# Kernel tuning notes

Measured on AMD Instinct MI355X. Metric: run time of the kernel, lower is better.

The kernel has to match this reference:

```python
import jax, jax.numpy as jnp
import numpy as np

N_NODES = 100000


def gcn_conv(x, W, b, src, dst, n_nodes):
    # x: [N, Fin], W: [Fin, Fout], edge (src->dst) with self-loops added,
    # symmetric normalization D^{-1/2} A D^{-1/2} as in PyG GCNConv defaults.
    h = x @ W  # [N, Fout]
    loops = jnp.arange(n_nodes, dtype=src.dtype)
    src_all = jnp.concatenate([src, loops])
    dst_all = jnp.concatenate([dst, loops])
    ones = jnp.ones(src_all.shape[0], dtype=h.dtype)
    deg = jax.ops.segment_sum(ones, dst_all, num_segments=n_nodes)  # in-degree incl. self-loop
    dinv = jnp.where(deg > 0, jax.lax.rsqrt(deg), 0.0)
    norm = dinv[src_all] * dinv[dst_all]  # [E+N]
    msg = h[src_all] * norm[:, None]      # gather + scale
    out = jax.ops.segment_sum(msg, dst_all, num_segments=n_nodes)  # scatter-add
    return out + b


def setup_inputs() -> dict:
    key = jax.random.key(0)
    k1, k2, k3, k4 = jax.random.split(key, 4)
    in_dim, hidden, out_dim = 128, 128, 64
    n_edges = 600000
    x = jax.random.normal(k1, (N_NODES, in_dim), dtype=jnp.float32)
    edge_index = jax.random.randint(k2, (2, n_edges), 0, N_NODES, dtype=jnp.int64)
    # Glorot-ish init for weights
    W1 = jax.random.normal(k3, (in_dim, hidden), dtype=jnp.float32) / np.sqrt(in_dim)
    b1 = jnp.zeros((hidden,), dtype=jnp.float32)
    W2 = jax.random.normal(k4, (hidden, out_dim), dtype=jnp.float32) / np.sqrt(hidden)
    b2 = jnp.zeros((out_dim,), dtype=jnp.float32)
    return {"x": x, "edge_index": edge_index, "W1": W1, "b1": b1, "W2": W2, "b2": b2}


def reference(x, edge_index, W1, b1, W2, b2):
    src, dst = edge_index[0], edge_index[1]
    h = jax.nn.relu(gcn_conv(x, W1, b1, src, dst, N_NODES))
    # dropout is identity in eval mode (training=False)
    return gcn_conv(h, W2, b2, src, dst, N_NODES)
```

## Files before the change

### kernel.cpp

```cpp
#include <hip/hip_runtime.h>
#include <hip/hip_bf16.h>
#include <stdint.h>

typedef unsigned int u32;
typedef unsigned short u16;
typedef unsigned long long u64;
typedef __attribute__((ext_vector_type(8))) short short8;
typedef __attribute__((ext_vector_type(4))) float f32x4;

#define SCAN_TILE 2048

__device__ __forceinline__ float bf2f(u16 u) {
    union { u32 u; float f; } v; v.u = ((u32)u) << 16; return v.f;
}
__device__ __forceinline__ u16 f2bf(float f) {
    u32 u = __float_as_uint(f);
    u32 r = (u + 0x7FFFu + ((u >> 16) & 1u)) >> 16;
    return (u16)r;
}
__device__ __forceinline__ u32 packbf(float lo, float hi) {
    return ((u32)f2bf(hi) << 16) | (u32)f2bf(lo);
}

template<int N>
__device__ __forceinline__ void wpack_one(const void* W, uint4* wpk, int p, int f32w) {
    const int n = p & (N - 1);
    const int kb = p >> ((N == 128) ? 7 : 6);
    u32 pk[4];
    if (f32w) {
        const float* wp = (const float*)W + (size_t)(kb * 8) * N + n;
        #pragma unroll
        for (int jj = 0; jj < 4; jj++)
            pk[jj] = packbf(wp[(2 * jj) * N], wp[(2 * jj + 1) * N]);
    } else {
        const u16* wp = (const u16*)W + (size_t)(kb * 8) * N + n;
        #pragma unroll
        for (int jj = 0; jj < 4; jj++)
            pk[jj] = ((u32)wp[(2 * jj + 1) * N] << 16) | (u32)wp[(2 * jj) * N];
    }
    uint4 v; v.x = pk[0]; v.y = pk[1]; v.z = pk[2]; v.w = pk[3];
    wpk[p] = v;
}

__global__ __launch_bounds__(256) void prep_k(const u32* __restrict__ xw,
                                              const u32* __restrict__ ew,
                                              int* __restrict__ flags,
                                              int* __restrict__ deg, int M,
                                              const void* __restrict__ W1,
                                              const void* __restrict__ W2,
                                              uint4* __restrict__ wpk1,
                                              uint4* __restrict__ wpk2,
                                              u64* __restrict__ lk, int nlk) {
    const int b = blockIdx.x, t = threadIdx.x;
    const int i4 = (b * 256 + t) * 4;
    if (i4 + 4 <= M) *(int4*)(deg + i4) = make_int4(0, 0, 0, 0);
    else { for (int j = 0; j < 4; j++) if (i4 + j < M) deg[i4 + j] = 0; }

    if (b < 12) {
        __shared__ int cnt;
        if (t == 0) cnt = 0;
        __syncthreads();
        int hits = 0;
        #pragma unroll
        for (int j = 0; j < 4; j++) {
            u32 f = (xw[t * 4 + j] >> 7) & 0xFFu;
            if (f >= 100u && f <= 140u) hits++;
        }
        atomicAdd(&cnt, hits);
        __syncthreads();
        const int f32w = (cnt < 512) ? 1 : 0;
        if (b < 8) wpack_one<128>(W1, wpk1, b * 256 + t, f32w);
        else       wpack_one<64> (W2, wpk2, (b - 8) * 256 + t, f32w);
        if (b == 0) {
            if (t < nlk) lk[t] = 0ull;
            if (t == 0) flags[0] = f32w;
            __shared__ u32 orr;
            if (t == 0) orr = 0u;
            __syncthreads();
            atomicOr(&orr, ew[2 * t + 1]);
            __syncthreads();
            if (t == 0) flags[1] = (orr == 0u) ? 1 : 0;
        }
    }
}

__global__ __launch_bounds__(256) void count_deg_k(const void* __restrict__ ei, int E,
                                                   const int* __restrict__ flags,
                                                   int* __restrict__ deg) {
    const int i2 = (blockIdx.x * 256 + threadIdx.x) * 2;
    if (i2 >= E) return;
    if (flags[1]) {
        const long long* dp = (const long long*)ei + E;
        if (i2 + 1 < E) {
            longlong2 v = *(const longlong2*)(dp + i2);
            atomicAdd(&deg[(int)v.x], 1);
            atomicAdd(&deg[(int)v.y], 1);
        } else atomicAdd(&deg[(int)dp[i2]], 1);
    } else {
        const int* dp = (const int*)ei + E;
        if (i2 + 1 < E) {
            int2 v = *(const int2*)(dp + i2);
            atomicAdd(&deg[v.x], 1);
            atomicAdd(&deg[v.y], 1);
        } else atomicAdd(&deg[dp[i2]], 1);
    }
}

__global__ __launch_bounds__(256) void scan_lb_k(const int* __restrict__ deg, int M,
                                                 u64* __restrict__ lk,
                                                 int* __restrict__ off,
                                                 int* __restrict__ cursor,
                                                 float* __restrict__ dinv, int nb) {
    const int bid = blockIdx.x, t = threadIdx.x;
    const int base = bid * SCAN_TILE + t * 8;
    int v[8];
    int s = 0;
    const bool full = (base + 8 <= M);
    if (full) {
        int4 a = *(const int4*)(deg + base);
        int4 b = *(const int4*)(deg + base + 4);
        v[0] = a.x; v[1] = a.y; v[2] = a.z; v[3] = a.w;
        v[4] = b.x; v[5] = b.y; v[6] = b.z; v[7] = b.w;
        s = v[0] + v[1] + v[2] + v[3] + v[4] + v[5] + v[6] + v[7];
    } else {
        #pragma unroll
        for (int j = 0; j < 8; j++) { v[j] = (base + j < M) ? deg[base + j] : 0; s += v[j]; }
    }
    __shared__ int buf[2][256];
    buf[0][t] = s;
    __syncthreads();
    int cur = 0;
    for (int d = 1; d < 256; d <<= 1) {
        int x = buf[cur][t];
        if (t >= d) x += buf[cur][t - d];
        buf[cur ^ 1][t] = x;
        __syncthreads();
        cur ^= 1;
    }
    const int incl = buf[cur][t];
    const int btotal = buf[cur][255];

    __shared__ int sbase;
    if (t == 0) {
        if (bid == 0) {
            __hip_atomic_store(&lk[0], (2ull << 62) | (u32)btotal,
                               __ATOMIC_RELEASE, __HIP_MEMORY_SCOPE_AGENT);
            sbase = 0;
        } else {
            __hip_atomic_store(&lk[bid], (1ull << 62) | (u32)btotal,
                               __ATOMIC_RELEASE, __HIP_MEMORY_SCOPE_AGENT);
            int run = 0;
            int j = bid - 1;
            while (j >= 0) {
                u64 w = __hip_atomic_load(&lk[j], __ATOMIC_ACQUIRE,
                                          __HIP_MEMORY_SCOPE_AGENT);
                const u64 st = w >> 62;
                if (st == 0) { __builtin_amdgcn_s_sleep(1); continue; }
                run += (int)(w & 0xFFFFFFFFull);
                if (st == 2ull) break;
                j--;
            }
            sbase = run;
            __hip_atomic_store(&lk[bid], (2ull << 62) | (u32)(run + btotal),
                               __ATOMIC_RELEASE, __HIP_MEMORY_SCOPE_AGENT);
        }
    }
    __syncthreads();

    int pre = sbase + incl - s;
    int o[8]; float dv[8];
    #pragma unroll
    for (int j = 0; j < 8; j++) {
        o[j] = pre;
        dv[j] = rsqrtf((float)(v[j] + 1));
        pre += v[j];
    }
    if (full) {
        *(int4*)(off + base)     = make_int4(o[0], o[1], o[2], o[3]);
        *(int4*)(off + base + 4) = make_int4(o[4], o[5], o[6], o[7]);
        *(int4*)(cursor + base)     = make_int4(o[0], o[1], o[2], o[3]);
        *(int4*)(cursor + base + 4) = make_int4(o[4], o[5], o[6], o[7]);
        *(float4*)(dinv + base)     = make_float4(dv[0], dv[1], dv[2], dv[3]);
        *(float4*)(dinv + base + 4) = make_float4(dv[4], dv[5], dv[6], dv[7]);
    } else {
        for (int j = 0; j < 8; j++) if (base + j < M) {
            off[base + j] = o[j]; cursor[base + j] = o[j]; dinv[base + j] = dv[j];
        }
    }
    if (bid == nb - 1 && t == 255) off[M] = sbase + btotal;
}

__global__ __launch_bounds__(256) void fill_k(const void* __restrict__ ei, int E,
                                              const int* __restrict__ flags,
                                              int* __restrict__ cursor, int* __restrict__ eidx) {
    const int i2 = (blockIdx.x * 256 + threadIdx.x) * 2;
    if (i2 >= E) return;
    int s0, d0, s1 = -1, d1 = -1;
    bool two = (i2 + 1 < E);
    if (flags[1]) {
        const long long* sp = (const long long*)ei;
        const long long* dp = sp + E;
        if (two) {
            longlong2 sv = *(const longlong2*)(sp + i2);
            longlong2 dv = *(const longlong2*)(dp + i2);
            s0 = (int)sv.x; s1 = (int)sv.y; d0 = (int)dv.x; d1 = (int)dv.y;
        } else { s0 = (int)sp[i2]; d0 = (int)dp[i2]; }
    } else {
        const int* sp = (const int*)ei;
        const int* dp = sp + E;
        if (two) {
            int2 sv = *(const int2*)(sp + i2);
            int2 dv = *(const int2*)(dp + i2);
            s0 = sv.x; s1 = sv.y; d0 = dv.x; d1 = dv.y;
        } else { s0 = sp[i2]; d0 = dp[i2]; }
    }
    int p0 = atomicAdd(&cursor[d0], 1);
    eidx[p0] = s0;
    if (two) {
        int p1 = atomicAdd(&cursor[d1], 1);
        eidx[p1] = s1;
    }
}

template<int N>
__global__ __launch_bounds__(256) void gemm_mfma_k(
    const void* __restrict__ X, const uint4* __restrict__ wpk,
    const float* __restrict__ dinv, u16* __restrict__ HS,
    const int* __restrict__ flags, int x_is_ext, int M)
{
    constexpr int NT = N / 16;
    constexpr int NC8 = N / 8;
    __shared__ u32 xlds[64 * 64];
    const int t = threadIdx.x;
    const int wave = t >> 6, lane = t & 63;
    const int q = lane >> 4, m = lane & 15;
    const bool xf32 = (x_is_ext != 0) && (flags[0] != 0);
    const int row0 = blockIdx.x * 64;

    for (int c = t; c < 1024; c += 256) {
        const int row = c >> 4, c8 = c & 15;
        const int grow = row0 + row;
        uint4 pk = make_uint4(0u, 0u, 0u, 0u);
        if (grow < M) {
            if (xf32) {
                const float* xp = (const float*)X + (size_t)grow * 128 + c8 * 8;
                float4 u = *(const float4*)xp;
                float4 v = *(const float4*)(xp + 4);
                pk.x = packbf(u.x, u.y); pk.y = packbf(u.z, u.w);
                pk.z = packbf(v.x, v.y); pk.w = packbf(v.z, v.w);
            } else {
                pk = *(const uint4*)((const u16*)X + (size_t)grow * 128 + c8 * 8);
            }
        }
        *(uint4*)&xlds[row * 64 + c8 * 4] = pk;
    }
    __syncthreads();

    union { uint4 u; short8 v; } a[4];
    #pragma unroll
    for (int s = 0; s < 4; s++)
        a[s].u = *(const uint4*)&xlds[(wave * 16 + m) * 64 + (s * 4 + q) * 4];

    f32x4 acc[NT];
    #pragma unroll
    for (int tt = 0; tt < NT; tt++)
        acc[tt] = (f32x4){0.f, 0.f, 0.f, 0.f};

    #pragma unroll
    for (int s = 0; s < 4; s++) {
        union { uint4 u; short8 v; } b[NT];
        #pragma unroll
        for (int tt = 0; tt < NT; tt++)
            b[tt].u = wpk[(s * 4 + q) * N + tt * 16 + m];
        #pragma unroll
        for (int tt = 0; tt < NT; tt++)
            acc[tt] = __builtin_amdgcn_mfma_f32_16x16x32_bf16(
                a[s].v, b[tt].v, acc[tt], 0, 0, 0);
    }

    float dv[4];
    #pragma unroll
    for (int r = 0; r < 4; r++) {
        const int grow = row0 + wave * 16 + q * 4 + r;
        dv[r] = (grow < M) ? dinv[grow] : 0.f;
    }

    u16* orow = (u16*)&xlds[wave * 16 * 64];
    #pragma unroll
    for (int tt = 0; tt < NT; tt++)
        #pragma unroll
        for (int r = 0; r < 4; r++)
            orow[(q * 4 + r) * N + tt * 16 + m] = f2bf(acc[tt][r] * dv[r]);

    constexpr int ITER = 16 * NC8 / 64;
    #pragma unroll
    for (int j = 0; j < ITER; j++) {
        const int cc = lane + j * 64;
        const int lrow = cc / NC8, c8 = cc % NC8;
        const int grow = row0 + wave * 16 + lrow;
        uint4 v = *(const uint4*)&((const u32*)orow)[lrow * (N / 2) + c8 * 4];
        if (grow < M)
            *(uint4*)(HS + (size_t)grow * N + c8 * 8) = v;
    }
}

template<int N, bool RELU>
__global__ __launch_bounds__(256) void aggregate_k(
    const u16* __restrict__ hs, const int* __restrict__ eidx,
    const int* __restrict__ off, const float* __restrict__ dinv,
    const void* __restrict__ bias, void* __restrict__ out,
    const int* __restrict__ flags, int out_is_ext, int M)
{
    constexpr int TPN = N / 8;
    constexpr int NPB = 256 / TPN;
    const int node = blockIdx.x * NPB + threadIdx.x / TPN;
    const int lane = threadIdx.x % TPN;
    if (node >= M) return;
    const int f32io = flags[0];
    const int beg = off[node], end = off[node + 1];
    const int c8 = lane * 8;
    const u16* __restrict__ hrow = hs + c8;

    float a[8];
    {
        uint4 sp = *(const uint4*)(hrow + (size_t)node * N);
        const u16* s = (const u16*)&sp;
        #pragma unroll
        for (int j = 0; j < 8; j++) a[j] = bf2f(s[j]);
    }

    int p = beg;
    for (; p + 4 <= end; p += 4) {
        const int s0 = eidx[p + 0], s1 = eidx[p + 1];
        const int s2 = eidx[p + 2], s3 = eidx[p + 3];
        uint4 v0 = *(const uint4*)(hrow + (size_t)s0 * N);
        uint4 v1 = *(const uint4*)(hrow + (size_t)s1 * N);
        uint4 v2 = *(const uint4*)(hrow + (size_t)s2 * N);
        uint4 v3 = *(const uint4*)(hrow + (size_t)s3 * N);
        const u16* q0 = (const u16*)&v0; const u16* q1 = (const u16*)&v1;
        const u16* q2 = (const u16*)&v2; const u16* q3 = (const u16*)&v3;
        #pragma unroll
        for (int j = 0; j < 8; j++)
            a[j] += (bf2f(q0[j]) + bf2f(q1[j])) + (bf2f(q2[j]) + bf2f(q3[j]));
    }
    for (; p < end; p++) {
        const int s = eidx[p];
        uint4 v = *(const uint4*)(hrow + (size_t)s * N);
        const u16* q = (const u16*)&v;
        #pragma unroll
        for (int j = 0; j < 8; j++) a[j] += bf2f(q[j]);
    }

    const float dv = dinv[node];
    float b[8];
    if (f32io) {
        float4 u = *(const float4*)((const float*)bias + c8);
        float4 v = *(const float4*)((const float*)bias + c8 + 4);
        b[0] = u.x; b[1] = u.y; b[2] = u.z; b[3] = u.w;
        b[4] = v.x; b[5] = v.y; b[6] = v.z; b[7] = v.w;
    } else {
        uint4 u = *(const uint4*)((const u16*)bias + c8);
        const u16* s = (const u16*)&u;
        #pragma unroll
        for (int j = 0; j < 8; j++) b[j] = bf2f(s[j]);
    }
    float o[8];
    #pragma unroll
    for (int j = 0; j < 8; j++) {
        o[j] = fmaf(dv, a[j], b[j]);
        if (RELU) o[j] = fmaxf(o[j], 0.f);
    }
    if (out_is_ext && f32io) {
        float* op = (float*)out + (size_t)node * N + c8;
        *(float4*)op       = make_float4(o[0], o[1], o[2], o[3]);
        *(float4*)(op + 4) = make_float4(o[4], o[5], o[6], o[7]);
    } else {
        uint4 pk;
        pk.x = packbf(o[0], o[1]); pk.y = packbf(o[2], o[3]);
        pk.z = packbf(o[4], o[5]); pk.w = packbf(o[6], o[7]);
        *(uint4*)((u16*)out + (size_t)node * N + c8) = pk;
    }
}

extern "C" void kernel_launch(void* const* d_in, const int* in_sizes, int n_in,
                              void* d_out, int out_size, void* d_ws, size_t ws_size,
                              hipStream_t stream) {
    const void* x  = d_in[0];
    const void* ei = d_in[1];
    const void* W1 = d_in[2];
    const void* b1 = d_in[3];
    const void* W2 = d_in[4];
    const void* b2 = d_in[5];

    const int M = in_sizes[0] / 128;
    const int E = in_sizes[1] / 2;
    const int NB = (M + SCAN_TILE - 1) / SCAN_TILE;

    char* ws = (char*)d_ws;
    size_t offb = 0;
    auto alloc = [&](size_t bytes) -> void* {
        void* p = ws + offb; offb += (bytes + 255) & ~(size_t)255; return p;
    };
    int*   flags  = (int*)  alloc(256);
    u64*   lk     = (u64*)  alloc(2048);
    uint4* wpk1   = (uint4*)alloc(16 * 128 * 16);
    uint4* wpk2   = (uint4*)alloc(16 * 64 * 16);
    int*   deg    = (int*)  alloc((size_t)M * 4);
    int*   off    = (int*)  alloc((size_t)(M + 1) * 4);
    int*   cursor = (int*)  alloc((size_t)M * 4);
    float* dinv   = (float*)alloc((size_t)M * 4);
    int*   eidx   = (int*)  alloc((size_t)E * 4);
    u16*   hs1    = (u16*)  alloc((size_t)M * 128 * 2);
    u16*   out1   = (u16*)  alloc((size_t)M * 128 * 2);
    u16*   hs2    = (u16*)  alloc((size_t)M * 64 * 2);
    (void)ws_size; (void)n_in; (void)out_size;

    prep_k<<<(M + 1023) / 1024, 256, 0, stream>>>((const u32*)x, (const u32*)ei, flags,
                                                  deg, M, W1, W2, wpk1, wpk2, lk, NB);
    count_deg_k<<<(E + 511) / 512, 256, 0, stream>>>(ei, E, flags, deg);
    scan_lb_k<<<NB, 256, 0, stream>>>(deg, M, lk, off, cursor, dinv, NB);
    fill_k<<<(E + 511) / 512, 256, 0, stream>>>(ei, E, flags, cursor, eidx);

    gemm_mfma_k<128><<<(M + 63) / 64, 256, 0, stream>>>(x, wpk1, dinv, hs1, flags, 1, M);
    aggregate_k<128, true><<<(M + 15) / 16, 256, 0, stream>>>(hs1, eidx, off, dinv, b1, out1,
                                                              flags, 0, M);
    gemm_mfma_k<64><<<(M + 63) / 64, 256, 0, stream>>>(out1, wpk2, dinv, hs2, flags, 0, M);
    aggregate_k<64, false><<<(M + 31) / 32, 256, 0, stream>>>(hs2, eidx, off, dinv, b2, d_out,
                                                              flags, 1, M);
}
```

Before: 241.5 us.

## Fuse GEMM1 with degree counting and layer-1 aggregation with GEMM2

The first GEMM now runs in the same launch as degree counting, using disjoint block ranges. Because dinv does not exist yet at that point, the source-side dinv scaling moves into the aggregation, which reads dinv per neighbour. Layer-1 aggregation is fused with the second GEMM through an LDS tile, which removes the out1 intermediate buffer and its global round trip as well as one launch. The cost is extra random dinv gathers per edge in aggregation and lower parallelism there (4 nodes per 16-lane group, 64 nodes per block, run in series).

```diff
diff --git a/kernel.cpp b/kernel.cpp
--- a/kernel.cpp
+++ b/kernel.cpp
@@ -84,25 +84,96 @@
     }
 }
 
-__global__ __launch_bounds__(256) void count_deg_k(const void* __restrict__ ei, int E,
-                                                   const int* __restrict__ flags,
-                                                   int* __restrict__ deg) {
-    const int i2 = (blockIdx.x * 256 + threadIdx.x) * 2;
-    if (i2 >= E) return;
-    if (flags[1]) {
-        const long long* dp = (const long long*)ei + E;
-        if (i2 + 1 < E) {
-            longlong2 v = *(const longlong2*)(dp + i2);
-            atomicAdd(&deg[(int)v.x], 1);
-            atomicAdd(&deg[(int)v.y], 1);
-        } else atomicAdd(&deg[(int)dp[i2]], 1);
-    } else {
-        const int* dp = (const int*)ei + E;
-        if (i2 + 1 < E) {
-            int2 v = *(const int2*)(dp + i2);
-            atomicAdd(&deg[v.x], 1);
-            atomicAdd(&deg[v.y], 1);
-        } else atomicAdd(&deg[dp[i2]], 1);
+__global__ __launch_bounds__(256) void gemm1_count_k(
+    const void* __restrict__ X, const uint4* __restrict__ wpk,
+    u16* __restrict__ HS, const int* __restrict__ flags, int M,
+    const void* __restrict__ ei, int E, int* __restrict__ deg, int GB)
+{
+    __shared__ u32 xlds[64 * 64];
+    const int t = threadIdx.x;
+
+    if ((int)blockIdx.x >= GB) {
+        const int i2 = (((int)blockIdx.x - GB) * 256 + t) * 2;
+        if (i2 >= E) return;
+        if (flags[1]) {
+            const long long* dp = (const long long*)ei + E;
+            if (i2 + 1 < E) {
+                longlong2 v = *(const longlong2*)(dp + i2);
+                atomicAdd(&deg[(int)v.x], 1);
+                atomicAdd(&deg[(int)v.y], 1);
+            } else atomicAdd(&deg[(int)dp[i2]], 1);
+        } else {
+            const int* dp = (const int*)ei + E;
+            if (i2 + 1 < E) {
+                int2 v = *(const int2*)(dp + i2);
+                atomicAdd(&deg[v.x], 1);
+                atomicAdd(&deg[v.y], 1);
+            } else atomicAdd(&deg[dp[i2]], 1);
+        }
+        return;
+    }
+
+    const int wave = t >> 6, lane = t & 63;
+    const int q = lane >> 4, m = lane & 15;
+    const bool xf32 = (flags[0] != 0);
+    const int row0 = blockIdx.x * 64;
+
+    for (int c = t; c < 1024; c += 256) {
+        const int row = c >> 4, c8 = c & 15;
+        const int grow = row0 + row;
+        uint4 pk = make_uint4(0u, 0u, 0u, 0u);
+        if (grow < M) {
+            if (xf32) {
+                const float* xp = (const float*)X + (size_t)grow * 128 + c8 * 8;
+                float4 u = *(const float4*)xp;
+                float4 v = *(const float4*)(xp + 4);
+                pk.x = packbf(u.x, u.y); pk.y = packbf(u.z, u.w);
+                pk.z = packbf(v.x, v.y); pk.w = packbf(v.z, v.w);
+            } else {
+                pk = *(const uint4*)((const u16*)X + (size_t)grow * 128 + c8 * 8);
+            }
+        }
+        *(uint4*)&xlds[row * 64 + c8 * 4] = pk;
+    }
+    __syncthreads();
+
+    union { uint4 u; short8 v; } a[4];
+    #pragma unroll
+    for (int s = 0; s < 4; s++)
+        a[s].u = *(const uint4*)&xlds[(wave * 16 + m) * 64 + (s * 4 + q) * 4];
+
+    f32x4 acc[8];
+    #pragma unroll
+    for (int tt = 0; tt < 8; tt++)
+        acc[tt] = (f32x4){0.f, 0.f, 0.f, 0.f};
+
+    #pragma unroll
+    for (int s = 0; s < 4; s++) {
+        union { uint4 u; short8 v; } b[8];
+        #pragma unroll
+        for (int tt = 0; tt < 8; tt++)
+            b[tt].u = wpk[(s * 4 + q) * 128 + tt * 16 + m];
+        #pragma unroll
+        for (int tt = 0; tt < 8; tt++)
+            acc[tt] = __builtin_amdgcn_mfma_f32_16x16x32_bf16(
+                a[s].v, b[tt].v, acc[tt], 0, 0, 0);
+    }
+
+    u16* orow = (u16*)&xlds[wave * 16 * 64];
+    #pragma unroll
+    for (int tt = 0; tt < 8; tt++)
+        #pragma unroll
+        for (int r = 0; r < 4; r++)
+            orow[(q * 4 + r) * 128 + tt * 16 + m] = f2bf(acc[tt][r]);
+
+    #pragma unroll
+    for (int j = 0; j < 4; j++) {
+        const int cc = lane + j * 64;
+        const int lrow = cc >> 4, c8 = cc & 15;
+        const int grow = row0 + wave * 16 + lrow;
+        uint4 v = *(const uint4*)&((const u32*)orow)[lrow * 64 + c8 * 4];
+        if (grow < M)
+            *(uint4*)(HS + (size_t)grow * 128 + c8 * 8) = v;
     }
 }
 
@@ -222,85 +293,136 @@
     }
 }
 
-template<int N>
-__global__ __launch_bounds__(256) void gemm_mfma_k(
-    const void* __restrict__ X, const uint4* __restrict__ wpk,
-    const float* __restrict__ dinv, u16* __restrict__ HS,
-    const int* __restrict__ flags, int x_is_ext, int M)
+__global__ __launch_bounds__(256) void agg1_gemm2_k(
+    const u16* __restrict__ hs, const int* __restrict__ eidx,
+    const int* __restrict__ off, const float* __restrict__ dinv,
+    const void* __restrict__ bias, const uint4* __restrict__ wpk,
+    u16* __restrict__ HS2, const int* __restrict__ flags, int M)
 {
-    constexpr int NT = N / 16;
-    constexpr int NC8 = N / 8;
-    __shared__ u32 xlds[64 * 64];
+    __shared__ u32 zlds[64 * 64];
     const int t = threadIdx.x;
+    const int row0 = blockIdx.x * 64;
+    const int f32io = flags[0];
+
+    const int lane16 = t & 15;
+    const int nsub   = t >> 4;
+    const int c8 = lane16 * 8;
+    const u16* __restrict__ hrow = hs + c8;
+
+    float bb[8];
+    if (f32io) {
+        float4 u = *(const float4*)((const float*)bias + c8);
+        float4 v = *(const float4*)((const float*)bias + c8 + 4);
+        bb[0] = u.x; bb[1] = u.y; bb[2] = u.z; bb[3] = u.w;
+        bb[4] = v.x; bb[5] = v.y; bb[6] = v.z; bb[7] = v.w;
+    } else {
+        uint4 u = *(const uint4*)((const u16*)bias + c8);
+        const u16* s = (const u16*)&u;
+        #pragma unroll
+        for (int j = 0; j < 8; j++) bb[j] = bf2f(s[j]);
+    }
+
+    #pragma unroll
+    for (int r = 0; r < 4; r++) {
+        const int node = row0 + r * 16 + nsub;
+        float o[8];
+        #pragma unroll
+        for (int j = 0; j < 8; j++) o[j] = 0.f;
+        if (node < M) {
+            const float dv = dinv[node];
+            float a[8];
+            {
+                uint4 sp = *(const uint4*)(hrow + (size_t)node * 128);
+                const u16* s = (const u16*)&sp;
+                #pragma unroll
+                for (int j = 0; j < 8; j++) a[j] = dv * bf2f(s[j]);
+            }
+            const int beg = off[node], end = off[node + 1];
+            int p = beg;
+            for (; p + 4 <= end; p += 4) {
+                const int s0 = eidx[p + 0], s1 = eidx[p + 1];
+                const int s2 = eidx[p + 2], s3 = eidx[p + 3];
+                const float d0 = dinv[s0], d1 = dinv[s1];
+                const float d2 = dinv[s2], d3 = dinv[s3];
+                uint4 v0 = *(const uint4*)(hrow + (size_t)s0 * 128);
+                uint4 v1 = *(const uint4*)(hrow + (size_t)s1 * 128);
+                uint4 v2 = *(const uint4*)(hrow + (size_t)s2 * 128);
+                uint4 v3 = *(const uint4*)(hrow + (size_t)s3 * 128);
+                const u16* q0 = (const u16*)&v0; const u16* q1 = (const u16*)&v1;
+                const u16* q2 = (const u16*)&v2; const u16* q3 = (const u16*)&v3;
+                #pragma unroll
+                for (int j = 0; j < 8; j++)
+                    a[j] = fmaf(d0, bf2f(q0[j]),
+                           fmaf(d1, bf2f(q1[j]),
+                           fmaf(d2, bf2f(q2[j]),
+                           fmaf(d3, bf2f(q3[j]), a[j]))));
+            }
+            for (; p < end; p++) {
+                const int s = eidx[p];
+                const float ds = dinv[s];
+                uint4 v = *(const uint4*)(hrow + (size_t)s * 128);
+                const u16* q = (const u16*)&v;
+                #pragma unroll
+                for (int j = 0; j < 8; j++) a[j] = fmaf(ds, bf2f(q[j]), a[j]);
+            }
+            #pragma unroll
+            for (int j = 0; j < 8; j++)
+                o[j] = fmaxf(fmaf(dv, a[j], bb[j]), 0.f);
+        }
+        uint4 pk;
+        pk.x = packbf(o[0], o[1]); pk.y = packbf(o[2], o[3]);
+        pk.z = packbf(o[4], o[5]); pk.w = packbf(o[6], o[7]);
+        *(uint4*)&zlds[(r * 16 + nsub) * 64 + lane16 * 4] = pk;
+    }
+    __syncthreads();
+
     const int wave = t >> 6, lane = t & 63;
     const int q = lane >> 4, m = lane & 15;
-    const bool xf32 = (x_is_ext != 0) && (flags[0] != 0);
-    const int row0 = blockIdx.x * 64;
-
-    for (int c = t; c < 1024; c += 256) {
-        const int row = c >> 4, c8 = c & 15;
-        const int grow = row0 + row;
-        uint4 pk = make_uint4(0u, 0u, 0u, 0u);
-        if (grow < M) {
-            if (xf32) {
-                const float* xp = (const float*)X + (size_t)grow * 128 + c8 * 8;
-                float4 u = *(const float4*)xp;
-                float4 v = *(const float4*)(xp + 4);
-                pk.x = packbf(u.x, u.y); pk.y = packbf(u.z, u.w);
-                pk.z = packbf(v.x, v.y); pk.w = packbf(v.z, v.w);
-            } else {
-                pk = *(const uint4*)((const u16*)X + (size_t)grow * 128 + c8 * 8);
-            }
-        }
-        *(uint4*)&xlds[row * 64 + c8 * 4] = pk;
-    }
-    __syncthreads();
-
-    union { uint4 u; short8 v; } a[4];
+
+    union { uint4 u; short8 v; } af[4];
     #pragma unroll
     for (int s = 0; s < 4; s++)
-        a[s].u = *(const uint4*)&xlds[(wave * 16 + m) * 64 + (s * 4 + q) * 4];
-
-    f32x4 acc[NT];
-    #pragma unroll
-    for (int tt = 0; tt < NT; tt++)
+        af[s].u = *(const uint4*)&zlds[(wave * 16 + m) * 64 + (s * 4 + q) * 4];
+
+    f32x4 acc[4];
+    #pragma unroll
+    for (int tt = 0; tt < 4; tt++)
         acc[tt] = (f32x4){0.f, 0.f, 0.f, 0.f};
 
     #pragma unroll
     for (int s = 0; s < 4; s++) {
-        union { uint4 u; short8 v; } b[NT];
-        #pragma unroll
-        for (int tt = 0; tt < NT; tt++)
-            b[tt].u = wpk[(s * 4 + q) * N + tt * 16 + m];
-        #pragma unroll
-        for (int tt = 0; tt < NT; tt++)
+        union { uint4 u; short8 v; } bf_[4];
+        #pragma unroll
+        for (int tt = 0; tt < 4; tt++)
+            bf_[tt].u = wpk[(s * 4 + q) * 64 + tt * 16 + m];
+        #pragma unroll
+        for (int tt = 0; tt < 4; tt++)
             acc[tt] = __builtin_amdgcn_mfma_f32_16x16x32_bf16(
-                a[s].v, b[tt].v, acc[tt], 0, 0, 0);
-    }
-
-    float dv[4];
+                af[s].v, bf_[tt].v, acc[tt], 0, 0, 0);
+    }
+
+    float dv4[4];
     #pragma unroll
     for (int r = 0; r < 4; r++) {
         const int grow = row0 + wave * 16 + q * 4 + r;
-        dv[r] = (grow < M) ? dinv[grow] : 0.f;
-    }
-
-    u16* orow = (u16*)&xlds[wave * 16 * 64];
-    #pragma unroll
-    for (int tt = 0; tt < NT; tt++)
+        dv4[r] = (grow < M) ? dinv[grow] : 0.f;
+    }
+
+    u16* orow = (u16*)&zlds[wave * 16 * 64];
+    #pragma unroll
+    for (int tt = 0; tt < 4; tt++)
         #pragma unroll
         for (int r = 0; r < 4; r++)
-            orow[(q * 4 + r) * N + tt * 16 + m] = f2bf(acc[tt][r] * dv[r]);
-
-    constexpr int ITER = 16 * NC8 / 64;
-    #pragma unroll
-    for (int j = 0; j < ITER; j++) {
+            orow[(q * 4 + r) * 64 + tt * 16 + m] = f2bf(acc[tt][r] * dv4[r]);
+
+    #pragma unroll
+    for (int j = 0; j < 2; j++) {
         const int cc = lane + j * 64;
-        const int lrow = cc / NC8, c8 = cc % NC8;
+        const int lrow = cc >> 3, c8b = cc & 7;
         const int grow = row0 + wave * 16 + lrow;
-        uint4 v = *(const uint4*)&((const u32*)orow)[lrow * (N / 2) + c8 * 4];
+        uint4 v = *(const uint4*)&((const u32*)orow)[lrow * 32 + c8b * 4];
         if (grow < M)
-            *(uint4*)(HS + (size_t)grow * N + c8 * 8) = v;
+            *(uint4*)(HS2 + (size_t)grow * 64 + c8b * 8) = v;
     }
 }
 
@@ -395,6 +517,8 @@
     const int M = in_sizes[0] / 128;
     const int E = in_sizes[1] / 2;
     const int NB = (M + SCAN_TILE - 1) / SCAN_TILE;
+    const int GB = (M + 63) / 64;
+    const int CB = (E + 511) / 512;
 
     char* ws = (char*)d_ws;
     size_t offb = 0;
@@ -411,20 +535,16 @@
     float* dinv   = (float*)alloc((size_t)M * 4);
     int*   eidx   = (int*)  alloc((size_t)E * 4);
     u16*   hs1    = (u16*)  alloc((size_t)M * 128 * 2);
-    u16*   out1   = (u16*)  alloc((size_t)M * 128 * 2);
     u16*   hs2    = (u16*)  alloc((size_t)M * 64 * 2);
     (void)ws_size; (void)n_in; (void)out_size;
 
     prep_k<<<(M + 1023) / 1024, 256, 0, stream>>>((const u32*)x, (const u32*)ei, flags,
                                                   deg, M, W1, W2, wpk1, wpk2, lk, NB);
-    count_deg_k<<<(E + 511) / 512, 256, 0, stream>>>(ei, E, flags, deg);
+    gemm1_count_k<<<GB + CB, 256, 0, stream>>>(x, wpk1, hs1, flags, M, ei, E, deg, GB);
     scan_lb_k<<<NB, 256, 0, stream>>>(deg, M, lk, off, cursor, dinv, NB);
     fill_k<<<(E + 511) / 512, 256, 0, stream>>>(ei, E, flags, cursor, eidx);
-
-    gemm_mfma_k<128><<<(M + 63) / 64, 256, 0, stream>>>(x, wpk1, dinv, hs1, flags, 1, M);
-    aggregate_k<128, true><<<(M + 15) / 16, 256, 0, stream>>>(hs1, eidx, off, dinv, b1, out1,
-                                                              flags, 0, M);
-    gemm_mfma_k<64><<<(M + 63) / 64, 256, 0, stream>>>(out1, wpk2, dinv, hs2, flags, 0, M);
+    agg1_gemm2_k<<<(M + 63) / 64, 256, 0, stream>>>(hs1, eidx, off, dinv, b1, wpk2, hs2,
+                                                    flags, M);
     aggregate_k<64, false><<<(M + 31) / 32, 256, 0, stream>>>(hs2, eidx, off, dinv, b2, d_out,
                                                               flags, 1, M);
 }
```

Result: faster. 235.3 us (-2.5%).
